# Kernel optimization log

Measured on AMD Instinct MI355X. Metric: run time of the kernel, lower is better.

Reference implementation:

```python
import jax, jax.numpy as jnp
import numpy as np

N, F, H, K, E = 10000, 128, 128, 500, 320000
EPS = 1e-15


def setup_inputs() -> dict:
    key = jax.random.key(0)
    ks = jax.random.split(key, 16)
    def lin(k, fi, fo):
        return jax.random.normal(k, (fi, fo), jnp.float32) / np.sqrt(fi).astype(np.float32)
    inp = {
        'nodes': jax.random.normal(ks[0], (N, F), jnp.float32),
        'edges': jax.random.randint(ks[1], (2, E), 0, N, jnp.int32),
        'batch': jnp.zeros((N,), jnp.int32),
        'W1': lin(ks[2], F, H), 'b1': jnp.zeros((H,), jnp.float32),
        'W2': lin(ks[3], H, H), 'b2': jnp.zeros((H,), jnp.float32),
        'pool_W': lin(ks[4], H, K), 'pool_b': jnp.zeros((K,), jnp.float32),
        'W3': lin(ks[5], H, H), 'b3': jnp.zeros((H,), jnp.float32),
        'W4': lin(ks[6], H, H), 'b4': jnp.zeros((H,), jnp.float32),
        'W5': lin(ks[7], H, F), 'b5': jnp.zeros((F,), jnp.float32),
    }
    return inp


def reference(nodes, edges, batch, W1, b1, W2, b2, pool_W, pool_b, W3, b3, W4, b4, W5, b5):
    n = nodes.shape[0]
    row, col = edges[0], edges[1]
    # GCN normalization with self-loops (computed once, shared by all convs)
    loop = jnp.arange(n, dtype=row.dtype)
    row_sl = jnp.concatenate([row, loop])
    col_sl = jnp.concatenate([col, loop])
    deg = jax.ops.segment_sum(jnp.ones_like(col_sl, dtype=nodes.dtype), col_sl, num_segments=n)
    dinv = jnp.where(deg > 0, 1.0 / jnp.sqrt(deg), 0.0)
    norm = dinv[row_sl] * dinv[col_sl]  # [E+N]

    def gcn(x, W, b):
        h = x @ W
        msg = h[row_sl] * norm[:, None]
        return jax.ops.segment_sum(msg, col_sl, num_segments=n) + b

    x = jnp.tanh(gcn(nodes, W1, b1))
    x = jnp.tanh(gcn(x, W2, b2))

    # dense batch (single graph) + dense adjacency [1, N, N]
    adj = jnp.zeros((n, n), x.dtype).at[row, col].add(1.0)[None]
    xd = x[None]                                   # [1, N, H]
    s_logits = xd @ pool_W + pool_b                # [1, N, K]

    # ---- dense_mincut_pool ----
    s = jax.nn.softmax(s_logits, axis=-1)
    k = s.shape[-1]
    out = jnp.einsum('bnk,bnh->bkh', s, xd)        # s^T x, [1, K, H]
    a_s = adj @ s                                  # [1, N, K]
    out_adj = jnp.swapaxes(s, 1, 2) @ a_s          # s^T A s, [1, K, K]
    mincut_num = jnp.trace(out_adj, axis1=1, axis2=2)
    d_flat = adj.sum(-1)                           # [1, N]
    # trace(s^T D s) = sum_n d_n * sum_k s_nk^2
    mincut_den = jnp.einsum('bn,bnk,bnk->b', d_flat, s, s) + EPS
    mincut_loss = jnp.mean(-(mincut_num / mincut_den))
    ss = jnp.swapaxes(s, 1, 2) @ s                 # [1, K, K]
    ss_norm = jnp.linalg.norm(ss, axis=(-1, -2), keepdims=True)
    i_s_normed = jnp.eye(k, dtype=ss.dtype) / jnp.sqrt(jnp.asarray(k, ss.dtype))
    ortho_loss = jnp.mean(jnp.linalg.norm(ss / (ss_norm + EPS) - i_s_normed, axis=(-1, -2)))
    # zero diagonal, then symmetric degree normalization
    out_adj = out_adj * (1.0 - jnp.eye(k, dtype=out_adj.dtype))
    d = jnp.sqrt(out_adj.sum(-1))[:, None] + EPS   # [1, 1, K]
    out_adj = out_adj / d / jnp.swapaxes(d, 1, 2)
    # ---- end pool ----

    s2 = jax.nn.softmax(s_logits, axis=-1)
    x_out = (s2 @ out)[0]                          # [N, H]
    adj_out = s2 @ (out_adj @ jnp.swapaxes(s2, 1, 2))  # [1, N, N]

    # recon_adj = False -> reuse original edge_index
    x = jnp.tanh(gcn(x_out, W3, b3))
    x = jnp.tanh(gcn(x, W4, b4))
    x = gcn(x, W5, b5)
    return x, adj_out, mincut_loss, ortho_loss
```

## Files before the change

kernel.cpp:

```cpp
#include <hip/hip_runtime.h>
#include <hip/hip_bf16.h>
#include <math.h>

#define EPSF 1e-15f

typedef __attribute__((ext_vector_type(8))) short bf16x8;
typedef __attribute__((ext_vector_type(4))) float f32x4;

__device__ __forceinline__ void gload_lds16(const void* g, void* l){
  __builtin_amdgcn_global_load_lds(
    (const __attribute__((address_space(1))) unsigned int*)(g),
    (__attribute__((address_space(3))) unsigned int*)(l), 16, 0, 0);
}

__device__ __forceinline__ float blo(unsigned v){ return __uint_as_float(v << 16); }
__device__ __forceinline__ float bhi(unsigned v){ return __uint_as_float(v & 0xFFFF0000u); }
__device__ __forceinline__ unsigned short b16(float v){
  __hip_bfloat16 b = __float2bfloat16(v);
  return *reinterpret_cast<unsigned short*>(&b);
}


__global__ void k_count_deg(const int* __restrict__ edges, int E, int* indeg, int* outdeg){
  int e = blockIdx.x*blockDim.x + threadIdx.x;
  if (e >= E) return;
  int r = edges[e], c = edges[E+e];
  atomicAdd(&outdeg[r], 1);
  atomicAdd(&indeg[c], 1);
}

__device__ __forceinline__ void scan_body(const int* cnt, int* rowptr, int* cur,
                                          float* dinvOut, int n){
  __shared__ int csum[257];
  const int T = 256;
  int chunk = (n + T - 1)/T;
  int t = threadIdx.x;
  int beg = t*chunk, end = min(n, beg + chunk);
  int s = 0;
  for (int i = beg; i < end; ++i) s += cnt[i];
  csum[t+1] = s;
  if (t == 0) csum[0] = 0;
  __syncthreads();
  if (t == 0){ for (int i = 1; i <= T; ++i) csum[i] += csum[i-1]; }
  __syncthreads();
  int acc = csum[t];
  for (int i = beg; i < end; ++i){
    rowptr[i] = acc;
    cur[i] = acc;
    if (dinvOut) dinvOut[i] = rsqrtf((float)(cnt[i] + 1));
    acc += cnt[i];
  }
  if (t == T-1) rowptr[n] = csum[T];
}

__global__ void k_scan_batch(const int* __restrict__ indeg, const int* __restrict__ outdeg,
                             int* rp_in, int* rp_out, int* cur_in, int* cur_out,
                             float* dinv, int n){
  if (blockIdx.x == 0) scan_body(indeg,  rp_in,  cur_in,  dinv,    n);
  else                 scan_body(outdeg, rp_out, cur_out, nullptr, n);
}

__global__ void k_fill_csr(const int* __restrict__ edges, int E, int* cur_in, int* cur_out,
                           int* __restrict__ src, int* __restrict__ dst){
  int e = blockIdx.x*blockDim.x + threadIdx.x;
  if (e >= E) return;
  int r = edges[e], c = edges[E+e];
  int p = atomicAdd(&cur_in[c], 1);  src[p] = r;
  int q = atomicAdd(&cur_out[r], 1); dst[q] = c;
}

__global__ __launch_bounds__(128)
void k_gcn_agg_v2(const __hip_bfloat16* __restrict__ hb, const float* __restrict__ dinv,
                  const int* __restrict__ rowptr, const int* __restrict__ src,
                  const float* __restrict__ bias, float* __restrict__ outf,
                  __hip_bfloat16* __restrict__ outb, int Hd4, int N, int do_tanh){
  int c = blockIdx.x*4 + (threadIdx.x >> 5);
  if (c >= N) return;
  int lane = threadIdx.x & 31;
  const uint2* h64 = (const uint2*)hb;
  float dc = dinv[c];
  uint2 vs = h64[(size_t)c*Hd4 + lane];
  float s0 = blo(vs.x)*dc, s1 = bhi(vs.x)*dc, s2 = blo(vs.y)*dc, s3 = bhi(vs.y)*dc;
  float t0 = 0.f, t1 = 0.f, t2 = 0.f, t3 = 0.f;
  int e0 = rowptr[c], e1 = rowptr[c+1];
  int e = e0;
  for (; e + 1 < e1; e += 2){
    int sa = src[e], sb = src[e+1];
    float da = dinv[sa], db = dinv[sb];
    uint2 va = h64[(size_t)sa*Hd4 + lane];
    uint2 vb = h64[(size_t)sb*Hd4 + lane];
    s0 += blo(va.x)*da; s1 += bhi(va.x)*da; s2 += blo(va.y)*da; s3 += bhi(va.y)*da;
    t0 += blo(vb.x)*db; t1 += bhi(vb.x)*db; t2 += blo(vb.y)*db; t3 += bhi(vb.y)*db;
  }
  if (e < e1){
    int sa = src[e];
    float da = dinv[sa];
    uint2 va = h64[(size_t)sa*Hd4 + lane];
    s0 += blo(va.x)*da; s1 += bhi(va.x)*da; s2 += blo(va.y)*da; s3 += bhi(va.y)*da;
  }
  s0 += t0; s1 += t1; s2 += t2; s3 += t3;
  float4 bb = ((const float4*)bias)[lane];
  float v0 = s0*dc + bb.x;
  float v1 = s1*dc + bb.y;
  float v2 = s2*dc + bb.z;
  float v3 = s3*dc + bb.w;
  if (do_tanh){ v0 = tanhf(v0); v1 = tanhf(v1); v2 = tanhf(v2); v3 = tanhf(v3); }
  if (outf){
    float4 o; o.x = v0; o.y = v1; o.z = v2; o.w = v3;
    ((float4*)(outf + (size_t)c*(Hd4*4)))[lane] = o;
  }
  if (outb){
    uint2 r;
    r.x = ((unsigned)b16(v1) << 16) | (unsigned)b16(v0);
    r.y = ((unsigned)b16(v3) << 16) | (unsigned)b16(v2);
    ((uint2*)(outb + (size_t)c*(Hd4*4)))[lane] = r;
  }
}

__global__ __launch_bounds__(128)
void k_as_agg_b4(const __hip_bfloat16* __restrict__ sb, const int* __restrict__ rowptr,
                 const int* __restrict__ dst, float* __restrict__ a_s,
                 int K, int K4, int KP4){
  int n = blockIdx.x;
  int e0 = rowptr[n], e1 = rowptr[n+1];
  const uint2* sb64 = (const uint2*)sb;
  for (int k = threadIdx.x; k < K4; k += blockDim.x){
    float a0 = 0.f, a1 = 0.f, a2 = 0.f, a3 = 0.f;
    for (int e = e0; e < e1; ++e){
      uint2 v = sb64[(size_t)dst[e]*KP4 + k];
      a0 += blo(v.x); a1 += bhi(v.x);
      a2 += blo(v.y); a3 += bhi(v.y);
    }
    ((f32x4*)(a_s + (size_t)n*K))[k] = (f32x4){a0, a1, a2, a3};
  }
}

__global__ void k_pack_bf16pad(const float* __restrict__ x, __hip_bfloat16* __restrict__ y,
                               int rows, int K, int KP){
  long long n = (long long)rows*KP;
  for (long long i = (long long)blockIdx.x*blockDim.x + threadIdx.x; i < n;
       i += (long long)gridDim.x*blockDim.x){
    int row = (int)(i / KP), col = (int)(i - (long long)row*KP);
    y[i] = (col < K) ? __float2bfloat16(x[(size_t)row*K + col]) : __float2bfloat16(0.f);
  }
}

__global__ void k_zero_pads(__hip_bfloat16* __restrict__ s_b, __hip_bfloat16* __restrict__ u_b,
                            int N, int K, int KP, int MP){
  int padc = KP - K;
  long long nA = (long long)N*padc;
  long long nB = (long long)(MP - N)*KP;
  long long tot = 2*(nA + nB);
  __hip_bfloat16 z = __float2bfloat16(0.f);
  for (long long i = (long long)blockIdx.x*blockDim.x + threadIdx.x; i < tot;
       i += (long long)gridDim.x*blockDim.x){
    long long j = i >> 1;
    __hip_bfloat16* buf = (i & 1) ? u_b : s_b;
    if (j < nA){
      int row = (int)(j / padc), col = K + (int)(j % padc);
      buf[(size_t)row*KP + col] = z;
    } else {
      buf[(size_t)N*KP + (j - nA)] = z;
    }
  }
}

__device__ __forceinline__ void transpose_tile(const float* X, __hip_bfloat16* XT,
                                               int R, int C, int Cp, int Np,
                                               int bx, int by){
  __shared__ float t[32][33];
  int jb = bx*32;
  int ib = by*32;
  int tx = threadIdx.x & 31, ty = threadIdx.x >> 5;
  #pragma unroll
  for (int k = 0; k < 4; ++k){
    int i = ib + ty + k*8, j = jb + tx;
    t[ty + k*8][tx] = (i < R && j < C) ? X[(size_t)i*C + j] : 0.f;
  }
  __syncthreads();
  #pragma unroll
  for (int k = 0; k < 4; ++k){
    int jr = jb + ty + k*8, ic = ib + tx;
    if (jr < Cp && ic < Np)
      XT[(size_t)jr*Np + ic] = __float2bfloat16(t[tx][ty + k*8]);
  }
}

__device__ __forceinline__ void transpose_tile_b(const __hip_bfloat16* X, __hip_bfloat16* XT,
                                                 int R, int C, int Cp, int Np,
                                                 int bx, int by){
  __shared__ float tb[32][33];
  int jb = bx*32;
  int ib = by*32;
  int tx = threadIdx.x & 31, ty = threadIdx.x >> 5;
  #pragma unroll
  for (int k = 0; k < 4; ++k){
    int i = ib + ty + k*8, j = jb + tx;
    tb[ty + k*8][tx] = (i < R && j < C) ? __bfloat162float(X[(size_t)i*C + j]) : 0.f;
  }
  __syncthreads();
  #pragma unroll
  for (int k = 0; k < 4; ++k){
    int jr = jb + ty + k*8, ic = ib + tx;
    if (jr < Cp && ic < Np)
      XT[(size_t)jr*Np + ic] = __float2bfloat16(tb[tx][ty + k*8]);
  }
}

struct TPar { const float* src; __hip_bfloat16* dst; int R, C, Cp, Np; };

__global__ __launch_bounds__(256)
void k_transpose_batch6(TPar p0, TPar p1, TPar p2, TPar p3, TPar p4, TPar p5){
  TPar p;
  switch (blockIdx.z){
    case 0: p = p0; break;
    case 1: p = p1; break;
    case 2: p = p2; break;
    case 3: p = p3; break;
    case 4: p = p4; break;
    default: p = p5; break;
  }
  if ((int)blockIdx.x >= (p.Cp + 31)/32 || (int)blockIdx.y >= (p.Np + 31)/32) return;
  transpose_tile(p.src, p.dst, p.R, p.C, p.Cp, p.Np, blockIdx.x, blockIdx.y);
}

__global__ __launch_bounds__(256)
void k_transpose_batch3(const float* __restrict__ s, __hip_bfloat16* __restrict__ st,
                        const float* __restrict__ a_s, __hip_bfloat16* __restrict__ a_st,
                        const __hip_bfloat16* __restrict__ xbb, __hip_bfloat16* __restrict__ xbt,
                        int N, int K, int KP, int Hd, int NP){
  int z = blockIdx.z;
  if (z < 2){
    transpose_tile(z ? a_s : s, z ? a_st : st, N, K, KP, NP, blockIdx.x, blockIdx.y);
  } else {
    if ((int)blockIdx.x*32 >= Hd) return;
    transpose_tile_b(xbb, xbt, N, Hd, Hd, NP, blockIdx.x, blockIdx.y);
  }
}

__global__ __launch_bounds__(256)
void k_transpose_ptop(const float* __restrict__ P, __hip_bfloat16* __restrict__ Pt,
                      const float* __restrict__ op, __hip_bfloat16* __restrict__ opT,
                      int K, int KP, int Hd){
  if (blockIdx.z == 0){
    transpose_tile(P, Pt, K, K, KP, KP, blockIdx.x, blockIdx.y);
  } else {
    if ((int)blockIdx.x*32 >= Hd) return;
    transpose_tile(op, opT, K, Hd, Hd, KP, blockIdx.x, blockIdx.y);
  }
}

#define MT 128
#define NT 128
__global__ __launch_bounds__(256)
void k_gemm_abt_mfma(const short* __restrict__ A, const short* __restrict__ B,
                     const float* __restrict__ bias,
                     float* __restrict__ Cf, __hip_bfloat16* __restrict__ Cb,
                     int M, int Nd, int KP, int ldcb, int swz){
  __shared__ __align__(16) short Asl[2*128*32];
  __shared__ __align__(16) short Bsl[2*128*32];
  int bx = blockIdx.x, by = blockIdx.y;
  if (swz){
    int gx = gridDim.x;
    int nwg = gx * gridDim.y;
    int bid = by*gx + bx;
    int q = nwg >> 3, r = nwg & 7;
    int xcd = bid & 7, o = bid >> 3;
    int nb = (xcd < r ? xcd*(q+1) : r*(q+1) + (xcd - r)*q) + o;
    bx = nb % gx; by = nb / gx;
  }
  int tid = threadIdx.x;
  int lane = tid & 63, wave = tid >> 6;
  int wr = wave >> 1, wc = wave & 1;
  int l15 = lane & 15, l4 = lane >> 4;
  int tM = by * MT, tN = bx * NT;

  f32x4 acc[4][4];
  #pragma unroll
  for (int i = 0; i < 4; ++i)
    #pragma unroll
    for (int j = 0; j < 4; ++j) acc[i][j] = (f32x4){0.f,0.f,0.f,0.f};

  int srow = tid >> 2, q2 = tid & 3;
  const short* gA0 = A + (size_t)(tM + srow)*KP + q2*8;
  const short* gA1 = A + (size_t)(tM + 64 + srow)*KP + q2*8;
  const short* gB0 = B + (size_t)(tN + srow)*KP + q2*8;
  const short* gB1 = B + (size_t)(tN + 64 + srow)*KP + q2*8;
  short* lA_0 = Asl + wave*512;
  short* lA_1 = Asl + 2048 + wave*512;
  short* lA_2 = Asl + 4096 + wave*512;
  short* lA_3 = Asl + 6144 + wave*512;
  short* lB_0 = Bsl + wave*512;
  short* lB_1 = Bsl + 2048 + wave*512;
  short* lB_2 = Bsl + 4096 + wave*512;
  short* lB_3 = Bsl + 6144 + wave*512;

  for (int k0 = 0; k0 < KP; k0 += 64){
    __syncthreads();
    gload_lds16(gA0 + k0,      lA_0);
    gload_lds16(gA1 + k0,      lA_1);
    gload_lds16(gA0 + k0 + 32, lA_2);
    gload_lds16(gA1 + k0 + 32, lA_3);
    gload_lds16(gB0 + k0,      lB_0);
    gload_lds16(gB1 + k0,      lB_1);
    gload_lds16(gB0 + k0 + 32, lB_2);
    gload_lds16(gB1 + k0 + 32, lB_3);
    __syncthreads();

    #pragma unroll
    for (int ks = 0; ks < 2; ++ks){
      bf16x8 af[4], bfr[4];
      #pragma unroll
      for (int mi = 0; mi < 4; ++mi)
        af[mi] = *(const bf16x8*)(Asl + ks*4096 + (wr*64 + mi*16 + l15)*32 + l4*8);
      #pragma unroll
      for (int nj = 0; nj < 4; ++nj)
        bfr[nj] = *(const bf16x8*)(Bsl + ks*4096 + (wc*64 + nj*16 + l15)*32 + l4*8);
      #pragma unroll
      for (int mi = 0; mi < 4; ++mi)
        #pragma unroll
        for (int nj = 0; nj < 4; ++nj)
          acc[mi][nj] = __builtin_amdgcn_mfma_f32_16x16x32_bf16(af[mi], bfr[nj], acc[mi][nj], 0, 0, 0);
    }
  }

  #pragma unroll
  for (int mi = 0; mi < 4; ++mi){
    #pragma unroll
    for (int r = 0; r < 4; ++r){
      int gr = tM + wr*64 + mi*16 + l4*4 + r;
      if (gr >= M) continue;
      #pragma unroll
      for (int nj = 0; nj < 4; ++nj){
        int gc = tN + wc*64 + nj*16 + l15;
        if (gc >= Nd) continue;
        float v = acc[mi][nj][r];
        if (bias) v += bias[gc];
        if (Cf) Cf[(size_t)gr*Nd + gc] = v;
        else    Cb[(size_t)gr*ldcb + gc] = __float2bfloat16(v);
      }
    }
  }
}

#define KT 32
__global__ __launch_bounds__(256)
void k_pool_sk(const short* __restrict__ st, const short* __restrict__ xbt,
               const short* __restrict__ a_st,
               float* __restrict__ out_pool, float* __restrict__ P, float* __restrict__ ssm,
               int K, int Hd, int KL, int kChunk){
  __shared__ __align__(16) short Asl[128*32];
  __shared__ __align__(16) short Bsl[128*32];
  int sel = blockIdx.z >> 3;
  int chunk = blockIdx.z & 7;
  const short* B = (sel == 0) ? xbt : (sel == 1) ? a_st : st;
  float* C = (sel == 0) ? out_pool : (sel == 1) ? P : ssm;
  int Nd = (sel == 0) ? Hd : K;
  if ((int)blockIdx.x * NT >= ((sel == 0) ? Hd : 512)) return;
  int tid = threadIdx.x;
  int lane = tid & 63, wave = tid >> 6;
  int wr = wave >> 1, wc = wave & 1;
  int l15 = lane & 15, l4 = lane >> 4;
  int tM = blockIdx.y * MT, tN = blockIdx.x * NT;
  int kBeg = chunk * kChunk;
  int kEnd = min(KL, kBeg + kChunk);

  f32x4 acc[4][4];
  #pragma unroll
  for (int i = 0; i < 4; ++i)
    #pragma unroll
    for (int j = 0; j < 4; ++j) acc[i][j] = (f32x4){0.f,0.f,0.f,0.f};

  const short* gA0 = st + (size_t)(tM + (tid>>2))*KL + (tid&3)*8;
  const short* gA1 = st + (size_t)(tM + 64 + (tid>>2))*KL + (tid&3)*8;
  const short* gB0 = B + (size_t)(tN + (tid>>2))*KL + (tid&3)*8;
  const short* gB1 = B + (size_t)(tN + 64 + (tid>>2))*KL + (tid&3)*8;
  short* lA0 = Asl + wave*512;
  short* lA1 = Asl + 2048 + wave*512;
  short* lB0 = Bsl + wave*512;
  short* lB1 = Bsl + 2048 + wave*512;

  for (int k0 = kBeg; k0 < kEnd; k0 += KT){
    __syncthreads();
    gload_lds16(gA0 + k0, lA0);
    gload_lds16(gA1 + k0, lA1);
    gload_lds16(gB0 + k0, lB0);
    gload_lds16(gB1 + k0, lB1);
    __syncthreads();

    bf16x8 af[4], bfr[4];
    #pragma unroll
    for (int mi = 0; mi < 4; ++mi)
      af[mi] = *(const bf16x8*)(Asl + (wr*64 + mi*16 + l15)*32 + l4*8);
    #pragma unroll
    for (int nj = 0; nj < 4; ++nj)
      bfr[nj] = *(const bf16x8*)(Bsl + (wc*64 + nj*16 + l15)*32 + l4*8);
    #pragma unroll
    for (int mi = 0; mi < 4; ++mi)
      #pragma unroll
      for (int nj = 0; nj < 4; ++nj)
        acc[mi][nj] = __builtin_amdgcn_mfma_f32_16x16x32_bf16(af[mi], bfr[nj], acc[mi][nj], 0, 0, 0);
  }

  #pragma unroll
  for (int mi = 0; mi < 4; ++mi){
    #pragma unroll
    for (int r = 0; r < 4; ++r){
      int gr = tM + wr*64 + mi*16 + l4*4 + r;
      if (gr >= K) continue;
      #pragma unroll
      for (int nj = 0; nj < 4; ++nj){
        int gc = tN + wc*64 + nj*16 + l15;
        if (gc >= Nd) continue;
        atomicAdd(&C[(size_t)gr*Nd + gc], acc[mi][nj][r]);
      }
    }
  }
}


__global__ __launch_bounds__(256)
void k_softmax(float* __restrict__ s, __hip_bfloat16* __restrict__ sb,
               const int* __restrict__ outdeg,
               float* __restrict__ scalars, int N, int K, int KP){
  int wid = threadIdx.x >> 6, lane = threadIdx.x & 63;
  int row = blockIdx.x*4 + wid;
  if (row >= N) return;
  float* sr = s + (size_t)row*K;
  __hip_bfloat16* sbr = sb + (size_t)row*KP;
  float v[8];
  float m = -INFINITY;
  #pragma unroll
  for (int i = 0; i < 8; ++i){
    int k = lane + i*64;
    v[i] = (k < K) ? sr[k] : -INFINITY;
    m = fmaxf(m, v[i]);
  }
  for (int off = 32; off; off >>= 1) m = fmaxf(m, __shfl_xor(m, off));
  float sum = 0.f;
  #pragma unroll
  for (int i = 0; i < 8; ++i){
    int k = lane + i*64;
    if (k < K){ v[i] = expf(v[i] - m); sum += v[i]; } else v[i] = 0.f;
  }
  for (int off = 32; off; off >>= 1) sum += __shfl_xor(sum, off);
  float inv = 1.f / sum;
  float ssq = 0.f;
  #pragma unroll
  for (int i = 0; i < 8; ++i){
    int k = lane + i*64;
    if (k < K){
      float p = v[i]*inv;
      sr[k] = p;
      sbr[k] = __float2bfloat16(p);
      ssq += p*p;
    }
  }
  for (int off = 32; off; off >>= 1) ssq += __shfl_xor(ssq, off);
  if (lane == 0) atomicAdd(&scalars[1], (float)outdeg[row] * ssq);
}

__global__ void k_stats1(const float* __restrict__ P, const float* __restrict__ ssm,
                         float* __restrict__ scalars, int K){
  float tr = 0.f, sq = 0.f;
  int n = K*K;
  for (int idx = blockIdx.x*blockDim.x + threadIdx.x; idx < n; idx += gridDim.x*blockDim.x){
    float v = ssm[idx]; sq += v*v;
    int i = idx / K, j = idx - i*K;
    if (i == j) tr += P[idx];
  }
  for (int off = 32; off; off >>= 1){
    tr += __shfl_xor(tr, off);
    sq += __shfl_xor(sq, off);
  }
  if ((threadIdx.x & 63) == 0){
    if (tr != 0.f) atomicAdd(&scalars[0], tr);
    atomicAdd(&scalars[2], sq);
  }
}

__global__ __launch_bounds__(256)
void k_rowsum_d(const float* __restrict__ P, float* __restrict__ dvec, int K){
  int wid = threadIdx.x >> 6, lane = threadIdx.x & 63;
  int row = blockIdx.x*4 + wid;
  if (row >= K) return;
  const float* pr = P + (size_t)row*K;
  float rs = 0.f;
  for (int j = lane; j < K; j += 64) if (j != row) rs += pr[j];
  for (int off = 32; off; off >>= 1) rs += __shfl_xor(rs, off);
  if (lane == 0) dvec[row] = sqrtf(rs) + EPSF;
}

__global__ void k_stats2(float* __restrict__ P, const float* __restrict__ ssm,
                         const float* __restrict__ dvec,
                         const float* __restrict__ scalars, float* __restrict__ out3, int K){
  float inv = 1.f / (sqrtf(scalars[2]) + EPSF);
  float isk = rsqrtf((float)K);
  float a = 0.f;
  int n = K*K;
  for (int idx = blockIdx.x*blockDim.x + threadIdx.x; idx < n; idx += gridDim.x*blockDim.x){
    int i = idx / K, j = idx - i*K;
    float v = ssm[idx]*inv - ((i == j) ? isk : 0.f);
    a += v*v;
    float pv = P[idx];
    P[idx] = (i == j) ? 0.f : pv / (dvec[i]*dvec[j]);
  }
  for (int off = 32; off; off >>= 1) a += __shfl_xor(a, off);
  if ((threadIdx.x & 63) == 0) atomicAdd(out3, a);
}

__global__ void k_finalize(const float* __restrict__ scalars, float* __restrict__ out2){
  if (threadIdx.x == 0){
    out2[0] = -(scalars[0] / (scalars[1] + EPSF));
    out2[1] = sqrtf(scalars[3]);
  }
}


extern "C" void kernel_launch(void* const* d_in, const int* in_sizes, int n_in,
                              void* d_out, int out_size, void* d_ws, size_t ws_size,
                              hipStream_t stream) {
  const float* nodes = (const float*)d_in[0];
  const int*   edges = (const int*)d_in[1];
  const float* W1 = (const float*)d_in[3];  const float* b1 = (const float*)d_in[4];
  const float* W2 = (const float*)d_in[5];  const float* b2 = (const float*)d_in[6];
  const float* pW = (const float*)d_in[7];  const float* pB = (const float*)d_in[8];
  const float* W3 = (const float*)d_in[9];  const float* b3 = (const float*)d_in[10];
  const float* W4 = (const float*)d_in[11]; const float* b4 = (const float*)d_in[12];
  const float* W5 = (const float*)d_in[13]; const float* b5 = (const float*)d_in[14];

  const int H = 128, F = 128, N = 10000, E = 320000, K = 500;
  const int KP = 512;
  const int NP = 10016;
  const int MP = 79*128;
  (void)n_in; (void)out_size; (void)in_sizes;

  float* out_x   = (float*)d_out;
  float* out_adj = out_x + (size_t)N*F;
  float* out_ls  = out_adj + (size_t)N*N;

  char* ws = (char*)d_ws;
  size_t off = 0;
  auto alloc = [&](size_t bytes) -> void* {
    off = (off + 255) & ~(size_t)255;
    void* p = ws + off;
    off += bytes;
    return p;
  };
  int*   deg2       = (int*)alloc((size_t)2*N*4);
  int*   indeg      = deg2;
  int*   outdeg     = deg2 + N;
  float* zf         = (float*)alloc(((size_t)K*H + 2*(size_t)K*K + 64)*4);
  float* out_pool   = zf;
  float* P          = zf + (size_t)K*H;
  float* ssm        = P + (size_t)K*K;
  float* scalars    = ssm + (size_t)K*K;
  __hip_bfloat16* s_b = (__hip_bfloat16*)alloc((size_t)MP*KP*2);
  __hip_bfloat16* u_b = (__hip_bfloat16*)alloc((size_t)MP*KP*2);
  int*   rowptr_in  = (int*)alloc((size_t)(N+1)*4);
  int*   rowptr_out = (int*)alloc((size_t)(N+1)*4);
  int*   cur_in     = (int*)alloc((size_t)N*4);
  int*   cur_out    = (int*)alloc((size_t)N*4);
  int*   csr_src    = (int*)alloc((size_t)E*4);
  int*   csr_dst    = (int*)alloc((size_t)E*4);
  float* dinv       = (float*)alloc((size_t)N*4);
  __hip_bfloat16* h_b  = (__hip_bfloat16*)alloc((size_t)N*H*2 + 32768);
  __hip_bfloat16* nodes_b = (__hip_bfloat16*)alloc((size_t)MP*H*2);
  __hip_bfloat16* xa_b = (__hip_bfloat16*)alloc((size_t)MP*H*2);
  __hip_bfloat16* xb_b = (__hip_bfloat16*)alloc((size_t)MP*H*2);
  float* s          = (float*)alloc((size_t)N*K*4);
  float* a_s        = (float*)alloc((size_t)N*K*4);
  float* dvec       = (float*)alloc((size_t)K*4);
  __hip_bfloat16* Pt_b = (__hip_bfloat16*)alloc((size_t)KP*KP*2);
  __hip_bfloat16* st_b = (__hip_bfloat16*)alloc((size_t)KP*NP*2);
  __hip_bfloat16* a_st = (__hip_bfloat16*)alloc((size_t)KP*NP*2);
  __hip_bfloat16* xbt  = (__hip_bfloat16*)alloc((size_t)H*NP*2);
  __hip_bfloat16* opT  = (__hip_bfloat16*)alloc((size_t)H*KP*2);
  __hip_bfloat16* W1t  = (__hip_bfloat16*)alloc((size_t)H*F*2);
  __hip_bfloat16* W2t  = (__hip_bfloat16*)alloc((size_t)H*H*2);
  __hip_bfloat16* W3t  = (__hip_bfloat16*)alloc((size_t)H*H*2);
  __hip_bfloat16* W4t  = (__hip_bfloat16*)alloc((size_t)H*H*2);
  __hip_bfloat16* W5t  = (__hip_bfloat16*)alloc((size_t)F*H*2);
  __hip_bfloat16* pWt  = (__hip_bfloat16*)alloc((size_t)KP*H*2);
  (void)ws_size;

  hipMemsetAsync(deg2, 0, (size_t)2*N*4, stream);
  hipMemsetAsync(zf,   0, ((size_t)K*H + 2*(size_t)K*K + 64)*4, stream);
  k_zero_pads<<<512, 256, 0, stream>>>(s_b, u_b, N, K, KP, MP);

  int eb = (E + 255)/256;
  k_count_deg<<<eb, 256, 0, stream>>>(edges, E, indeg, outdeg);
  k_scan_batch<<<2, 256, 0, stream>>>(indeg, outdeg, rowptr_in, rowptr_out,
                                      cur_in, cur_out, dinv, N);
  k_fill_csr<<<eb, 256, 0, stream>>>(edges, E, cur_in, cur_out, csr_src, csr_dst);

  {
    TPar p0 = { W1, W1t, F, H, H, F };
    TPar p1 = { W2, W2t, H, H, H, H };
    TPar p2 = { W3, W3t, H, H, H, H };
    TPar p3 = { W4, W4t, H, H, H, H };
    TPar p4 = { W5, W5t, H, F, F, H };
    TPar p5 = { pW, pWt, H, K, KP, H };
    dim3 g(16, 4, 6);
    k_transpose_batch6<<<g, 256, 0, stream>>>(p0, p1, p2, p3, p4, p5);
  }
  k_pack_bf16pad<<<1024, 256, 0, stream>>>(nodes, nodes_b, N, F, F);

  auto mfma = [&](const __hip_bfloat16* A, const __hip_bfloat16* B, const float* bias,
                  float* Cf, __hip_bfloat16* Cb, int M, int Nd, int Kp, int ldcb, int swz){
    dim3 g((Nd + NT - 1)/NT, (M + MT - 1)/MT);
    k_gemm_abt_mfma<<<g, 256, 0, stream>>>((const short*)A, (const short*)B, bias,
                                           Cf, Cb, M, Nd, Kp, ldcb, swz);
  };

  mfma(nodes_b, W1t, nullptr, nullptr, h_b, N, H, F, H, 0);
  k_gcn_agg_v2<<<(N+3)/4, 128, 0, stream>>>(h_b, dinv, rowptr_in, csr_src, b1, nullptr, xa_b, H/4, N, 1);
  mfma(xa_b, W2t, nullptr, nullptr, h_b, N, H, H, H, 0);
  k_gcn_agg_v2<<<(N+3)/4, 128, 0, stream>>>(h_b, dinv, rowptr_in, csr_src, b2, nullptr, xb_b, H/4, N, 1);

  mfma(xb_b, pWt, pB, s, nullptr, N, K, H, 0, 0);
  k_softmax<<<(N+3)/4, 256, 0, stream>>>(s, s_b, outdeg, scalars, N, K, KP);
  k_as_agg_b4<<<N, 128, 0, stream>>>(s_b, rowptr_out, csr_dst, a_s, K, K/4, KP/4);
  { dim3 g(KP/32, NP/32, 3); k_transpose_batch3<<<g, 256, 0, stream>>>(s, st_b, a_s, a_st,
                                                                       xb_b, xbt, N, K, KP, H, NP); }
  const int kChunk = 1280;
  { dim3 g(4, 4, 24); k_pool_sk<<<g, 256, 0, stream>>>((const short*)st_b, (const short*)xbt,
                                                       (const short*)a_st,
                                                       out_pool, P, ssm, K, H, NP, kChunk); }
  k_stats1<<<128, 256, 0, stream>>>(P, ssm, scalars, K);
  k_rowsum_d<<<(K+3)/4, 256, 0, stream>>>(P, dvec, K);
  k_stats2<<<128, 256, 0, stream>>>(P, ssm, dvec, scalars, &scalars[3], K);
  k_finalize<<<1, 64, 0, stream>>>(scalars, out_ls);

  { dim3 g(16, 16, 2); k_transpose_ptop<<<g, 256, 0, stream>>>(P, Pt_b, out_pool, opT, K, KP, H); }
  mfma(s_b, Pt_b, nullptr, nullptr, u_b, N, K, KP, KP, 0);
  mfma(u_b, s_b, nullptr, out_adj, nullptr, N, N, KP, 0, 1);
  mfma(s_b, opT, nullptr, nullptr, xa_b, N, H, KP, H, 0);

  mfma(xa_b, W3t, nullptr, nullptr, h_b, N, H, H, H, 0);
  k_gcn_agg_v2<<<(N+3)/4, 128, 0, stream>>>(h_b, dinv, rowptr_in, csr_src, b3, nullptr, xb_b, H/4, N, 1);
  mfma(xb_b, W4t, nullptr, nullptr, h_b, N, H, H, H, 0);
  k_gcn_agg_v2<<<(N+3)/4, 128, 0, stream>>>(h_b, dinv, rowptr_in, csr_src, b4, nullptr, xa_b, H/4, N, 1);
  mfma(xa_b, W5t, nullptr, nullptr, h_b, N, F, H, F, 0);
  k_gcn_agg_v2<<<(N+3)/4, 128, 0, stream>>>(h_b, dinv, rowptr_in, csr_src, b5, out_x, nullptr, F/4, N, 0);
}
```

Measured before the change: 857.0 us.

## Add 256x256-tile MFMA GEMM for the dense NxN adjacency output

Adds a dedicated 512-thread kernel with 256x256 output tiles and XCD-aware block remapping for the large u·s^T GEMM that writes the N×N adj_out matrix. The generic 128x128 GEMM drops its swizzle option and goes back from a 64-wide to a 32-wide K step per iteration. The larger tile is meant to raise reuse of A and B and cut global and L2 traffic on the dominant GEMM. The cost is more registers and LDS per block and fewer blocks in flight, and MP padding grows to 80 tiles so the 256-row tiles stay in bounds.

```diff
diff --git a/kernel.cpp b/kernel.cpp
--- a/kernel.cpp
+++ b/kernel.cpp
@@ -252,23 +252,15 @@
 
 #define MT 128
 #define NT 128
+#define KT 32
 __global__ __launch_bounds__(256)
 void k_gemm_abt_mfma(const short* __restrict__ A, const short* __restrict__ B,
                      const float* __restrict__ bias,
                      float* __restrict__ Cf, __hip_bfloat16* __restrict__ Cb,
-                     int M, int Nd, int KP, int ldcb, int swz){
-  __shared__ __align__(16) short Asl[2*128*32];
-  __shared__ __align__(16) short Bsl[2*128*32];
+                     int M, int Nd, int KP, int ldcb){
+  __shared__ __align__(16) short Asl[128*32];
+  __shared__ __align__(16) short Bsl[128*32];
   int bx = blockIdx.x, by = blockIdx.y;
-  if (swz){
-    int gx = gridDim.x;
-    int nwg = gx * gridDim.y;
-    int bid = by*gx + bx;
-    int q = nwg >> 3, r = nwg & 7;
-    int xcd = bid & 7, o = bid >> 3;
-    int nb = (xcd < r ? xcd*(q+1) : r*(q+1) + (xcd - r)*q) + o;
-    bx = nb % gx; by = nb / gx;
-  }
   int tid = threadIdx.x;
   int lane = tid & 63, wave = tid >> 6;
   int wr = wave >> 1, wc = wave & 1;
@@ -281,47 +273,35 @@
     #pragma unroll
     for (int j = 0; j < 4; ++j) acc[i][j] = (f32x4){0.f,0.f,0.f,0.f};
 
-  int srow = tid >> 2, q2 = tid & 3;
-  const short* gA0 = A + (size_t)(tM + srow)*KP + q2*8;
-  const short* gA1 = A + (size_t)(tM + 64 + srow)*KP + q2*8;
-  const short* gB0 = B + (size_t)(tN + srow)*KP + q2*8;
-  const short* gB1 = B + (size_t)(tN + 64 + srow)*KP + q2*8;
-  short* lA_0 = Asl + wave*512;
-  short* lA_1 = Asl + 2048 + wave*512;
-  short* lA_2 = Asl + 4096 + wave*512;
-  short* lA_3 = Asl + 6144 + wave*512;
-  short* lB_0 = Bsl + wave*512;
-  short* lB_1 = Bsl + 2048 + wave*512;
-  short* lB_2 = Bsl + 4096 + wave*512;
-  short* lB_3 = Bsl + 6144 + wave*512;
-
-  for (int k0 = 0; k0 < KP; k0 += 64){
+  const short* gA0 = A + (size_t)(tM + (tid>>2))*KP + (tid&3)*8;
+  const short* gA1 = A + (size_t)(tM + 64 + (tid>>2))*KP + (tid&3)*8;
+  const short* gB0 = B + (size_t)(tN + (tid>>2))*KP + (tid&3)*8;
+  const short* gB1 = B + (size_t)(tN + 64 + (tid>>2))*KP + (tid&3)*8;
+  short* lA0 = Asl + wave*512;
+  short* lA1 = Asl + 2048 + wave*512;
+  short* lB0 = Bsl + wave*512;
+  short* lB1 = Bsl + 2048 + wave*512;
+
+  for (int k0 = 0; k0 < KP; k0 += KT){
     __syncthreads();
-    gload_lds16(gA0 + k0,      lA_0);
-    gload_lds16(gA1 + k0,      lA_1);
-    gload_lds16(gA0 + k0 + 32, lA_2);
-    gload_lds16(gA1 + k0 + 32, lA_3);
-    gload_lds16(gB0 + k0,      lB_0);
-    gload_lds16(gB1 + k0,      lB_1);
-    gload_lds16(gB0 + k0 + 32, lB_2);
-    gload_lds16(gB1 + k0 + 32, lB_3);
+    gload_lds16(gA0 + k0, lA0);
+    gload_lds16(gA1 + k0, lA1);
+    gload_lds16(gB0 + k0, lB0);
+    gload_lds16(gB1 + k0, lB1);
     __syncthreads();
 
-    #pragma unroll
-    for (int ks = 0; ks < 2; ++ks){
-      bf16x8 af[4], bfr[4];
-      #pragma unroll
-      for (int mi = 0; mi < 4; ++mi)
-        af[mi] = *(const bf16x8*)(Asl + ks*4096 + (wr*64 + mi*16 + l15)*32 + l4*8);
+    bf16x8 af[4], bfr[4];
+    #pragma unroll
+    for (int mi = 0; mi < 4; ++mi)
+      af[mi] = *(const bf16x8*)(Asl + (wr*64 + mi*16 + l15)*32 + l4*8);
+    #pragma unroll
+    for (int nj = 0; nj < 4; ++nj)
+      bfr[nj] = *(const bf16x8*)(Bsl + (wc*64 + nj*16 + l15)*32 + l4*8);
+    #pragma unroll
+    for (int mi = 0; mi < 4; ++mi)
       #pragma unroll
       for (int nj = 0; nj < 4; ++nj)
-        bfr[nj] = *(const bf16x8*)(Bsl + ks*4096 + (wc*64 + nj*16 + l15)*32 + l4*8);
-      #pragma unroll
-      for (int mi = 0; mi < 4; ++mi)
-        #pragma unroll
-        for (int nj = 0; nj < 4; ++nj)
-          acc[mi][nj] = __builtin_amdgcn_mfma_f32_16x16x32_bf16(af[mi], bfr[nj], acc[mi][nj], 0, 0, 0);
-    }
+        acc[mi][nj] = __builtin_amdgcn_mfma_f32_16x16x32_bf16(af[mi], bfr[nj], acc[mi][nj], 0, 0, 0);
   }
 
   #pragma unroll
@@ -343,7 +323,78 @@
   }
 }
 
-#define KT 32
+__global__ __launch_bounds__(512)
+void k_gemm_abt_mfma256(const short* __restrict__ A, const short* __restrict__ B,
+                        float* __restrict__ Cf, int M, int Nd, int KP){
+  __shared__ __align__(16) short Asl[256*32];
+  __shared__ __align__(16) short Bsl[256*32];
+  int gx = gridDim.x;
+  int nwg = gx * gridDim.y;
+  int bid = blockIdx.y*gx + blockIdx.x;
+  int q = nwg >> 3, r = nwg & 7;
+  int xcd = bid & 7, o = bid >> 3;
+  int nb = (xcd < r ? xcd*(q+1) : r*(q+1) + (xcd - r)*q) + o;
+  int bx = nb % gx, by = nb / gx;
+
+  int tid = threadIdx.x;
+  int lane = tid & 63, wave = tid >> 6;
+  int wr = wave >> 2, wc = wave & 3;
+  int l15 = lane & 15, l4 = lane >> 4;
+  int tM = by * 256, tN = bx * 256;
+
+  f32x4 acc[8][4];
+  #pragma unroll
+  for (int i = 0; i < 8; ++i)
+    #pragma unroll
+    for (int j = 0; j < 4; ++j) acc[i][j] = (f32x4){0.f,0.f,0.f,0.f};
+
+  int srow = wave*16 + (lane >> 2), q2 = lane & 3;
+  const short* gA0 = A + (size_t)(tM + srow)*KP + q2*8;
+  const short* gA1 = A + (size_t)(tM + 128 + srow)*KP + q2*8;
+  const short* gB0 = B + (size_t)(tN + srow)*KP + q2*8;
+  const short* gB1 = B + (size_t)(tN + 128 + srow)*KP + q2*8;
+  short* lA0 = Asl + wave*512;
+  short* lA1 = Asl + 4096 + wave*512;
+  short* lB0 = Bsl + wave*512;
+  short* lB1 = Bsl + 4096 + wave*512;
+
+  for (int k0 = 0; k0 < KP; k0 += KT){
+    __syncthreads();
+    gload_lds16(gA0 + k0, lA0);
+    gload_lds16(gA1 + k0, lA1);
+    gload_lds16(gB0 + k0, lB0);
+    gload_lds16(gB1 + k0, lB1);
+    __syncthreads();
+
+    bf16x8 af[8], bfr[4];
+    #pragma unroll
+    for (int mi = 0; mi < 8; ++mi)
+      af[mi] = *(const bf16x8*)(Asl + (wr*128 + mi*16 + l15)*32 + l4*8);
+    #pragma unroll
+    for (int nj = 0; nj < 4; ++nj)
+      bfr[nj] = *(const bf16x8*)(Bsl + (wc*64 + nj*16 + l15)*32 + l4*8);
+    #pragma unroll
+    for (int mi = 0; mi < 8; ++mi)
+      #pragma unroll
+      for (int nj = 0; nj < 4; ++nj)
+        acc[mi][nj] = __builtin_amdgcn_mfma_f32_16x16x32_bf16(af[mi], bfr[nj], acc[mi][nj], 0, 0, 0);
+  }
+
+  #pragma unroll
+  for (int mi = 0; mi < 8; ++mi){
+    #pragma unroll
+    for (int r = 0; r < 4; ++r){
+      int gr = tM + wr*128 + mi*16 + l4*4 + r;
+      if (gr >= M) continue;
+      #pragma unroll
+      for (int nj = 0; nj < 4; ++nj){
+        int gc = tN + wc*64 + nj*16 + l15;
+        if (gc < Nd) Cf[(size_t)gr*Nd + gc] = acc[mi][nj][r];
+      }
+    }
+  }
+}
+
 __global__ __launch_bounds__(256)
 void k_pool_sk(const short* __restrict__ st, const short* __restrict__ xbt,
                const short* __restrict__ a_st,
@@ -532,7 +583,7 @@
   const int H = 128, F = 128, N = 10000, E = 320000, K = 500;
   const int KP = 512;
   const int NP = 10016;
-  const int MP = 79*128;
+  const int MP = 80*128;
   (void)n_in; (void)out_size; (void)in_sizes;
 
   float* out_x   = (float*)d_out;
@@ -607,18 +658,18 @@
   k_pack_bf16pad<<<1024, 256, 0, stream>>>(nodes, nodes_b, N, F, F);
 
   auto mfma = [&](const __hip_bfloat16* A, const __hip_bfloat16* B, const float* bias,
-                  float* Cf, __hip_bfloat16* Cb, int M, int Nd, int Kp, int ldcb, int swz){
+                  float* Cf, __hip_bfloat16* Cb, int M, int Nd, int Kp, int ldcb){
     dim3 g((Nd + NT - 1)/NT, (M + MT - 1)/MT);
     k_gemm_abt_mfma<<<g, 256, 0, stream>>>((const short*)A, (const short*)B, bias,
-                                           Cf, Cb, M, Nd, Kp, ldcb, swz);
+                                           Cf, Cb, M, Nd, Kp, ldcb);
   };
 
-  mfma(nodes_b, W1t, nullptr, nullptr, h_b, N, H, F, H, 0);
+  mfma(nodes_b, W1t, nullptr, nullptr, h_b, N, H, F, H);
   k_gcn_agg_v2<<<(N+3)/4, 128, 0, stream>>>(h_b, dinv, rowptr_in, csr_src, b1, nullptr, xa_b, H/4, N, 1);
-  mfma(xa_b, W2t, nullptr, nullptr, h_b, N, H, H, H, 0);
+  mfma(xa_b, W2t, nullptr, nullptr, h_b, N, H, H, H);
   k_gcn_agg_v2<<<(N+3)/4, 128, 0, stream>>>(h_b, dinv, rowptr_in, csr_src, b2, nullptr, xb_b, H/4, N, 1);
 
-  mfma(xb_b, pWt, pB, s, nullptr, N, K, H, 0, 0);
+  mfma(xb_b, pWt, pB, s, nullptr, N, K, H, 0);
   k_softmax<<<(N+3)/4, 256, 0, stream>>>(s, s_b, outdeg, scalars, N, K, KP);
   k_as_agg_b4<<<N, 128, 0, stream>>>(s_b, rowptr_out, csr_dst, a_s, K, K/4, KP/4);
   { dim3 g(KP/32, NP/32, 3); k_transpose_batch3<<<g, 256, 0, stream>>>(s, st_b, a_s, a_st,
@@ -633,14 +684,18 @@
   k_finalize<<<1, 64, 0, stream>>>(scalars, out_ls);
 
   { dim3 g(16, 16, 2); k_transpose_ptop<<<g, 256, 0, stream>>>(P, Pt_b, out_pool, opT, K, KP, H); }
-  mfma(s_b, Pt_b, nullptr, nullptr, u_b, N, K, KP, KP, 0);
-  mfma(u_b, s_b, nullptr, out_adj, nullptr, N, N, KP, 0, 1);
-  mfma(s_b, opT, nullptr, nullptr, xa_b, N, H, KP, H, 0);
-
-  mfma(xa_b, W3t, nullptr, nullptr, h_b, N, H, H, H, 0);
+  mfma(s_b, Pt_b, nullptr, nullptr, u_b, N, K, KP, KP);
+  {
+    dim3 g(40, 40);
+    k_gemm_abt_mfma256<<<g, 512, 0, stream>>>((const short*)u_b, (const short*)s_b,
+                                              out_adj, N, N, KP);
+  }
+  mfma(s_b, opT, nullptr, nullptr, xa_b, N, H, KP, H);
+
+  mfma(xa_b, W3t, nullptr, nullptr, h_b, N, H, H, H);
   k_gcn_agg_v2<<<(N+3)/4, 128, 0, stream>>>(h_b, dinv, rowptr_in, csr_src, b3, nullptr, xb_b, H/4, N, 1);
-  mfma(xb_b, W4t, nullptr, nullptr, h_b, N, H, H, H, 0);
+  mfma(xb_b, W4t, nullptr, nullptr, h_b, N, H, H, H);
   k_gcn_agg_v2<<<(N+3)/4, 128, 0, stream>>>(h_b, dinv, rowptr_in, csr_src, b4, nullptr, xa_b, H/4, N, 1);
-  mfma(xa_b, W5t, nullptr, nullptr, h_b, N, F, H, F, 0);
+  mfma(xa_b, W5t, nullptr, nullptr, h_b, N, F, H, F);
   k_gcn_agg_v2<<<(N+3)/4, 128, 0, stream>>>(h_b, dinv, rowptr_in, csr_src, b5, out_x, nullptr, F/4, N, 0);
 }
```

Measured after the change: 823.0 us. -4.0%, faster.
